# Optimization experiments

Hardware: AMD Instinct MI355X
Metric: run time of the kernel (lower is better)

## Reference

```python
import jax, jax.numpy as jnp
import numpy as np

NEG_SLOPE = 0.2  # PyG GATConv default LeakyReLU slope


def gat_layer(x, src, dst, W, a_src, a_dst, bias, num_nodes, heads, out_ch, concat):
    # x: [N, in], W: [in, heads*out_ch], a_src/a_dst: [heads, out_ch]
    h = (x @ W).reshape(num_nodes, heads, out_ch)          # [N,H,C]
    alpha_s = jnp.sum(h * a_src, axis=-1)                  # [N,H]
    alpha_d = jnp.sum(h * a_dst, axis=-1)                  # [N,H]
    e = jax.nn.leaky_relu(alpha_s[src] + alpha_d[dst], NEG_SLOPE)  # [E,H]
    # softmax over incoming edges of each destination node
    e_max = jax.ops.segment_max(e, dst, num_segments=num_nodes)   # [N,H]
    e_exp = jnp.exp(e - e_max[dst])                        # [E,H]
    denom = jax.ops.segment_sum(e_exp, dst, num_segments=num_nodes)  # [N,H]
    alpha = e_exp / denom[dst]                             # [E,H]
    msg = h[src] * alpha[:, :, None]                       # [E,H,C]
    out = jax.ops.segment_sum(msg, dst, num_segments=num_nodes)     # [N,H,C]
    if concat:
        out = out.reshape(num_nodes, heads * out_ch)
    else:
        out = out.mean(axis=1)
    return out + bias


def setup_inputs() -> dict:
    key = jax.random.key(0)
    ks = jax.random.split(key, 12)
    N, E = 50000, 800000
    IN, HID, OUT, H = 128, 32, 64, 4
    x = jax.random.normal(ks[0], (N, IN), dtype=jnp.float32)
    edge_index = jax.random.randint(ks[1], (2, E), 0, N, dtype=jnp.int32)
    s = 1.0 / np.sqrt(IN)
    W1 = jax.random.normal(ks[2], (IN, H * HID), dtype=jnp.float32) * s
    a_src1 = jax.random.normal(ks[3], (H, HID), dtype=jnp.float32) * 0.1
    a_dst1 = jax.random.normal(ks[4], (H, HID), dtype=jnp.float32) * 0.1
    b1 = jnp.zeros((H * HID,), dtype=jnp.float32)
    s2 = 1.0 / np.sqrt(H * HID)
    W2 = jax.random.normal(ks[5], (H * HID, OUT), dtype=jnp.float32) * s2
    a_src2 = jax.random.normal(ks[6], (1, OUT), dtype=jnp.float32) * 0.1
    a_dst2 = jax.random.normal(ks[7], (1, OUT), dtype=jnp.float32) * 0.1
    b2 = jnp.zeros((OUT,), dtype=jnp.float32)
    return {"x": x, "edge_index": edge_index, "W1": W1, "a_src1": a_src1,
            "a_dst1": a_dst1, "b1": b1, "W2": W2, "a_src2": a_src2,
            "a_dst2": a_dst2, "b2": b2}


def reference(x, edge_index, W1, a_src1, a_dst1, b1, W2, a_src2, a_dst2, b2):
    N = x.shape[0]
    src, dst = edge_index[0], edge_index[1]
    h = gat_layer(x, src, dst, W1, a_src1, a_dst1, b1, N, heads=4, out_ch=32, concat=True)
    h = jax.nn.elu(h)
    # dropout is identity in eval / p=0.0
    out = gat_layer(h, src, dst, W2, a_src2, a_dst2, b2, N, heads=1, out_ch=64, concat=False)
    return out
```

## Files before the change

### kernel.cpp

```cpp
#include <hip/hip_runtime.h>

#define C1 128
#define C2 64
#define CAP 96

typedef __attribute__((ext_vector_type(8))) _Float16 half8;
typedef __attribute__((ext_vector_type(2))) _Float16 half2v;
typedef __attribute__((ext_vector_type(2))) __fp16  fp16x2;
typedef __attribute__((ext_vector_type(4))) float floatx4;

__device__ __forceinline__ float lrelu(float v) { return v > 0.f ? v : 0.2f * v; }

__device__ __forceinline__ unsigned pk2h(float a, float b) {
    union { fp16x2 p; unsigned u; } c;
    c.p = __builtin_amdgcn_cvt_pkrtz(a, b);
    return c.u;
}

__global__ __launch_bounds__(256)
void gemm1_mfma_kernel(const float* __restrict__ x, const float* __restrict__ W1,
                       const float* __restrict__ asrc, const float* __restrict__ adst,
                       unsigned* __restrict__ h1d,
                       float* __restrict__ as1, float* __restrict__ ad1,
                       int* __restrict__ cursor, int N) {
    for (int i = blockIdx.x * 256 + threadIdx.x; i < N; i += gridDim.x * 256)
        cursor[i] = 0;

    __shared__ __align__(16) unsigned short Bs[128 * 136];
    for (int i = threadIdx.x; i < 128 * 64; i += 256) {
        int col = i & 127;
        int k = (i >> 7) * 2;
        *(unsigned*)&Bs[col * 136 + k] = pk2h(W1[k * 128 + col], W1[(k + 1) * 128 + col]);
    }
    __syncthreads();

    const int lane = threadIdx.x & 63, ww = threadIdx.x >> 6;
    const int quad = lane >> 4, l16 = lane & 15;
    const int nodeBase = blockIdx.x * 64 + ww * 16;
    int arow = nodeBase + l16;
    if (arow >= N) arow = N - 1;
    const float* xp = x + (size_t)arow * C1 + quad * 8;
    half8 afr[4];
#pragma unroll
    for (int kk = 0; kk < 4; ++kk) {
        float4 a0 = *(const float4*)(xp + kk * 32);
        float4 a1 = *(const float4*)(xp + kk * 32 + 4);
        union { half8 v; unsigned u[4]; } fr;
        fr.u[0] = pk2h(a0.x, a0.y);
        fr.u[1] = pk2h(a0.z, a0.w);
        fr.u[2] = pk2h(a1.x, a1.y);
        fr.u[3] = pk2h(a1.z, a1.w);
        afr[kk] = fr.v;
    }

#pragma unroll
    for (int h = 0; h < 4; ++h) {
        floatx4 accL = {0.f, 0.f, 0.f, 0.f};
        floatx4 accH = {0.f, 0.f, 0.f, 0.f};
        const int colL = h * 32 + l16;
        const int colH = colL + 16;
        const unsigned short* bL = &Bs[colL * 136 + quad * 8];
        const unsigned short* bH = &Bs[colH * 136 + quad * 8];
#pragma unroll
        for (int kk = 0; kk < 4; ++kk) {
            half8 bfrL = *(const half8*)(bL + kk * 32);
            half8 bfrH = *(const half8*)(bH + kk * 32);
            accL = __builtin_amdgcn_mfma_f32_16x16x32_f16(afr[kk], bfrL, accL, 0, 0, 0);
            accH = __builtin_amdgcn_mfma_f32_16x16x32_f16(afr[kk], bfrH, accH, 0, 0, 0);
        }
#pragma unroll
        for (int reg = 0; reg < 4; ++reg) {
            int node = nodeBase + quad * 4 + reg;
            if (node < N) h1d[(size_t)node * 64 + h * 16 + l16] = pk2h(accL[reg], accH[reg]);
        }
        float avL = asrc[colL], dvL = adst[colL];
        float avH = asrc[colH], dvH = adst[colH];
#pragma unroll
        for (int reg = 0; reg < 4; ++reg) {
            float ts = accL[reg] * avL + accH[reg] * avH;
            float td = accL[reg] * dvL + accH[reg] * dvH;
#pragma unroll
            for (int o = 1; o < 16; o <<= 1) {
                ts += __shfl_xor(ts, o, 64);
                td += __shfl_xor(td, o, 64);
            }
            if (l16 == 0) {
                int node = nodeBase + quad * 4 + reg;
                if (node < N) {
                    as1[node * 4 + h] = ts;
                    ad1[node * 4 + h] = td;
                }
            }
        }
    }
}

__global__ __launch_bounds__(256)
void fill_kernel(const int* __restrict__ ei, int* __restrict__ cursor,
                 int* __restrict__ csrc, int N, int E) {
    const int part = blockIdx.x & 7;
    const int bIdx = blockIdx.x >> 3;
    const int bpp  = gridDim.x >> 3;
    const int lo = (int)(((long)N * part) >> 3);
    const int hi = (int)(((long)N * (part + 1)) >> 3);

    const int E4 = ((E & 3) == 0) ? (E >> 2) : 0;
    const int4* d4 = (const int4*)(ei + E);
    const int4* s4 = (const int4*)ei;
    for (int q = bIdx * 256 + threadIdx.x; q < E4; q += bpp * 256) {
        int4 dv = d4[q];
        int4 sv = s4[q];
        int dd[4] = {dv.x, dv.y, dv.z, dv.w};
        int ss[4] = {sv.x, sv.y, sv.z, sv.w};
        int pos[4];
        bool act[4];
#pragma unroll
        for (int i = 0; i < 4; ++i) {
            act[i] = (dd[i] >= lo) & (dd[i] < hi) & ((unsigned)ss[i] < (unsigned)N);
            pos[i] = act[i] ? atomicAdd(&cursor[dd[i]], 1) : 0;
        }
#pragma unroll
        for (int i = 0; i < 4; ++i)
            if (act[i] && pos[i] < CAP) csrc[dd[i] * CAP + pos[i]] = ss[i];
    }
    for (int e = E4 * 4 + bIdx * 256 + threadIdx.x; e < E; e += bpp * 256) {
        int dd = ei[E + e];
        if (dd < lo || dd >= hi) continue;
        int ss = ei[e];
        if ((unsigned)ss >= (unsigned)N) continue;
        int pp = atomicAdd(&cursor[dd], 1);
        if (pp < CAP) csrc[dd * CAP + pp] = ss;
    }
}

__global__ __launch_bounds__(256)
void msg1_csr_kernel(const int* __restrict__ cursor, const int* __restrict__ csrc,
                     const unsigned* __restrict__ h1u, const float* __restrict__ as1,
                     const float* __restrict__ ad1, const float* __restrict__ b1,
                     unsigned* __restrict__ out1, int N) {
    __shared__ float ws[4][64];
    const int wid = threadIdx.x >> 6;
    const int d = blockIdx.x * 4 + wid;
    if (d >= N) return;
    const int lane = threadIdx.x & 63;
    const int e16 = lane & 15;
    const int head = lane >> 4;
    int dg = cursor[d]; if (dg > CAP) dg = CAP;
    const int base = d * CAP;
    const float wadh = ad1[d * 4 + head];
    float accx = 0.f, accy = 0.f, sumw = 0.f;
    for (int jj = 0; jj < dg; jj += 16) {
        int idx = jj + e16;
        if (idx >= dg) idx = dg - 1;
        const int myS = csrc[base + idx];
        unsigned rv[16];
#pragma unroll
        for (int k = 0; k < 16; ++k) {
            int s = __builtin_amdgcn_readlane(myS, k);
            rv[k] = h1u[(unsigned)s * 64u + (unsigned)lane];
        }
        float w = 0.f;
        if (jj + e16 < dg)
            w = __expf(lrelu(as1[myS * 4 + head] + wadh));
        ws[wid][lane] = w;
#pragma unroll
        for (int j = 0; j < 4; ++j) {
            float4 wf = ((const float4*)&ws[wid][head * 16])[j];
            union { unsigned u; half2v p; } c0, c1, c2, c3;
            c0.u = rv[4 * j + 0]; c1.u = rv[4 * j + 1];
            c2.u = rv[4 * j + 2]; c3.u = rv[4 * j + 3];
            sumw += (wf.x + wf.y) + (wf.z + wf.w);
            accx += wf.x * (float)c0.p[0]; accy += wf.x * (float)c0.p[1];
            accx += wf.y * (float)c1.p[0]; accy += wf.y * (float)c1.p[1];
            accx += wf.z * (float)c2.p[0]; accy += wf.z * (float)c2.p[1];
            accx += wf.w * (float)c3.p[0]; accy += wf.w * (float)c3.p[1];
        }
    }
    float inv = (sumw > 0.f) ? 1.f / sumw : 0.f;
    float rx = accx * inv + b1[32 * head + e16];
    float ry = accy * inv + b1[32 * head + e16 + 16];
    rx = rx > 0.f ? rx : expm1f(rx);
    ry = ry > 0.f ? ry : expm1f(ry);
    out1[(size_t)d * 64 + lane] = pk2h(rx, ry);
}

__global__ __launch_bounds__(256)
void gemm2_mfma_kernel(const unsigned short* __restrict__ h2, const float* __restrict__ W2,
                       const float* __restrict__ asrc, const float* __restrict__ adst,
                       unsigned* __restrict__ g2d, float* __restrict__ as2,
                       float* __restrict__ ad2, int N) {
    __shared__ __align__(16) unsigned short Bs[64 * 136];
    for (int i = threadIdx.x; i < 64 * 64; i += 256) {
        int col = i & 63;
        int p = i >> 6;
        int k0 = 32 * (p >> 4) + (p & 15);
        *(unsigned*)&Bs[col * 136 + 2 * p] = pk2h(W2[k0 * 64 + col], W2[(k0 + 16) * 64 + col]);
    }
    __syncthreads();

    const int lane = threadIdx.x & 63, ww = threadIdx.x >> 6;
    const int quad = lane >> 4, l16 = lane & 15;
    const int nodeBase = blockIdx.x * 64 + ww * 16;
    int arow = nodeBase + l16;
    if (arow >= N) arow = N - 1;
    const unsigned short* xp = h2 + (size_t)arow * C1 + quad * 8;
    half8 afr[4];
#pragma unroll
    for (int kk = 0; kk < 4; ++kk)
        afr[kk] = *(const half8*)(xp + kk * 32);

    float sacc[4] = {0.f,0.f,0.f,0.f}, dacc[4] = {0.f,0.f,0.f,0.f};
#pragma unroll
    for (int ctp = 0; ctp < 2; ++ctp) {
        floatx4 accL = {0.f, 0.f, 0.f, 0.f};
        floatx4 accH = {0.f, 0.f, 0.f, 0.f};
        const int colL = ctp * 16 + l16;
        const int colH = colL + 32;
        const unsigned short* bL = &Bs[colL * 136 + quad * 8];
        const unsigned short* bH = &Bs[colH * 136 + quad * 8];
#pragma unroll
        for (int kk = 0; kk < 4; ++kk) {
            half8 bfrL = *(const half8*)(bL + kk * 32);
            half8 bfrH = *(const half8*)(bH + kk * 32);
            accL = __builtin_amdgcn_mfma_f32_16x16x32_f16(afr[kk], bfrL, accL, 0, 0, 0);
            accH = __builtin_amdgcn_mfma_f32_16x16x32_f16(afr[kk], bfrH, accH, 0, 0, 0);
        }
#pragma unroll
        for (int reg = 0; reg < 4; ++reg) {
            int node = nodeBase + quad * 4 + reg;
            if (node < N) g2d[(size_t)node * 32 + colL] = pk2h(accL[reg], accH[reg]);
        }
        float avL = asrc[colL], dvL = adst[colL];
        float avH = asrc[colH], dvH = adst[colH];
#pragma unroll
        for (int reg = 0; reg < 4; ++reg) {
            sacc[reg] += accL[reg] * avL + accH[reg] * avH;
            dacc[reg] += accL[reg] * dvL + accH[reg] * dvH;
        }
    }
#pragma unroll
    for (int reg = 0; reg < 4; ++reg) {
        float ts = sacc[reg], td = dacc[reg];
#pragma unroll
        for (int o = 1; o < 16; o <<= 1) {
            ts += __shfl_xor(ts, o, 64);
            td += __shfl_xor(td, o, 64);
        }
        if (l16 == 0) {
            int node = nodeBase + quad * 4 + reg;
            if (node < N) { as2[node] = ts; ad2[node] = td; }
        }
    }
}

__global__ __launch_bounds__(256)
void msg2_csr_kernel(const int* __restrict__ cursor, const int* __restrict__ csrc,
                     const unsigned* __restrict__ g2u, const float* __restrict__ as2,
                     const float* __restrict__ ad2, const float* __restrict__ b2,
                     float* __restrict__ yf, int N) {
    __shared__ float wsm[4][32];
    __shared__ int   ssm[4][32];
    const int wid = threadIdx.x >> 6;
    const int d = blockIdx.x * 4 + wid;
    if (d >= N) return;
    const int lane = threadIdx.x & 63;
    const int half = lane >> 5;
    const int l32 = lane & 31;
    int dg = cursor[d]; if (dg > CAP) dg = CAP;
    const int base = d * CAP;
    const float add = ad2[d];
    float accx = 0.f, accy = 0.f, sumw = 0.f;
    for (int jj = 0; jj < dg; jj += 32) {
        int idx = jj + l32;
        if (idx >= dg) idx = dg - 1;
        const int myS = csrc[base + idx];
        float w = 0.f;
        if (jj + l32 < dg) w = __expf(lrelu(as2[myS] + add));
        ssm[wid][l32] = myS;
        wsm[wid][l32] = w;
        int4 s0 = ((const int4*)&ssm[wid][half * 16])[0];
        int4 s1 = ((const int4*)&ssm[wid][half * 16])[1];
        int4 s2 = ((const int4*)&ssm[wid][half * 16])[2];
        int4 s3 = ((const int4*)&ssm[wid][half * 16])[3];
        int ss[16] = {s0.x, s0.y, s0.z, s0.w, s1.x, s1.y, s1.z, s1.w,
                      s2.x, s2.y, s2.z, s2.w, s3.x, s3.y, s3.z, s3.w};
        unsigned rv[16];
#pragma unroll
        for (int k = 0; k < 16; ++k)
            rv[k] = g2u[(unsigned)ss[k] * 32u + (unsigned)l32];
#pragma unroll
        for (int j = 0; j < 4; ++j) {
            float4 wf = ((const float4*)&wsm[wid][half * 16])[j];
            union { unsigned u; half2v p; } c0, c1, c2, c3;
            c0.u = rv[4 * j + 0]; c1.u = rv[4 * j + 1];
            c2.u = rv[4 * j + 2]; c3.u = rv[4 * j + 3];
            sumw += (wf.x + wf.y) + (wf.z + wf.w);
            accx += wf.x * (float)c0.p[0]; accy += wf.x * (float)c0.p[1];
            accx += wf.y * (float)c1.p[0]; accy += wf.y * (float)c1.p[1];
            accx += wf.z * (float)c2.p[0]; accy += wf.z * (float)c2.p[1];
            accx += wf.w * (float)c3.p[0]; accy += wf.w * (float)c3.p[1];
        }
    }
    accx += __shfl_xor(accx, 32, 64);
    accy += __shfl_xor(accy, 32, 64);
    sumw += __shfl_xor(sumw, 32, 64);
    if (half == 0) {
        float inv = (sumw > 0.f) ? 1.f / sumw : 0.f;
        yf[(size_t)d * 64 + l32]      = accx * inv + b2[l32];
        yf[(size_t)d * 64 + 32 + l32] = accy * inv + b2[l32 + 32];
    }
}

extern "C" void kernel_launch(void* const* d_in, const int* in_sizes, int n_in,
                              void* d_out, int out_size, void* d_ws, size_t ws_size,
                              hipStream_t stream) {
    const float* x    = (const float*)d_in[0];
    const int*   ei   = (const int*)d_in[1];
    const float* W1   = (const float*)d_in[2];
    const float* a_s1 = (const float*)d_in[3];
    const float* a_d1 = (const float*)d_in[4];
    const float* b1   = (const float*)d_in[5];
    const float* W2   = (const float*)d_in[6];
    const float* a_s2 = (const float*)d_in[7];
    const float* a_d2 = (const float*)d_in[8];
    const float* b2   = (const float*)d_in[9];

    const int N = in_sizes[0] / C1;
    const int E = in_sizes[1] / 2;

    auto align16 = [](size_t v) { return (v + 15) & ~(size_t)15; };
    const size_t RF   = 16;
    const size_t RCUR = align16((size_t)N * 4);
    const size_t RSRC = align16((size_t)N * CAP * 4);
    const size_t R1   = align16((size_t)N * C1 * 4);
    const size_t R2   = align16((size_t)N * 8 * 4);

    char* base = (char*)d_ws;
    int*  cursor = (int*)(base + RF);
    int*  csrc   = (int*)(base + RF + RCUR);
    char* R1p = base + RF + RCUR + RSRC;
    char* R2p = R1p + R1;
    char* R4p = R2p + R2;
    (void)ws_size;

    unsigned* h1 = (unsigned*)R1p;
    unsigned* g2 = (unsigned*)R1p;
    float* as1 = (float*)R2p;
    float* ad1 = as1 + (size_t)N * 4;
    float* as2 = (float*)R2p;
    float* ad2 = as2 + N;
    unsigned* out1 = (unsigned*)R4p;

    const int nbTile = (N + 63) / 64;
    const int nbWave4 = (N + 3) / 4;

    gemm1_mfma_kernel<<<nbTile, 256, 0, stream>>>(x, W1, a_s1, a_d1, h1, as1, ad1, cursor, N);
    fill_kernel<<<2048, 256, 0, stream>>>(ei, cursor, csrc, N, E);
    msg1_csr_kernel<<<nbWave4, 256, 0, stream>>>(cursor, csrc, (const unsigned*)h1,
        as1, ad1, b1, out1, N);
    gemm2_mfma_kernel<<<nbTile, 256, 0, stream>>>((const unsigned short*)out1, W2,
        a_s2, a_d2, g2, as2, ad2, N);
    msg2_csr_kernel<<<nbWave4, 256, 0, stream>>>(cursor, csrc, (const unsigned*)g2,
        as2, ad2, b2, (float*)d_out, N);
}
```

Baseline: 226.1 us.

## Fuse layer-2 projection into msg1 kernel using fdot2 and shared W2

Removes the separate gemm2 MFMA kernel and computes each node's 64-wide layer-2 projection plus attention logits at the end of msg1, using packed half dot products against a swizzled W2 table in shared memory. This avoids writing and re-reading the intermediate hidden features and one kernel launch. In exchange every 4-node block re-stages and converts all of W2 into LDS, adding global loads and shared memory pressure, and the matmul moves from MFMA to scalar fdot2.

```diff
diff --git a/kernel.cpp b/kernel.cpp
--- a/kernel.cpp
+++ b/kernel.cpp
@@ -15,6 +15,9 @@
     union { fp16x2 p; unsigned u; } c;
     c.p = __builtin_amdgcn_cvt_pkrtz(a, b);
     return c.u;
+}
+__device__ __forceinline__ half2v u2h(unsigned v) {
+    union { unsigned u; half2v h; } c; c.u = v; return c.h;
 }
 
 __global__ __launch_bounds__(256)
@@ -137,8 +140,22 @@
 void msg1_csr_kernel(const int* __restrict__ cursor, const int* __restrict__ csrc,
                      const unsigned* __restrict__ h1u, const float* __restrict__ as1,
                      const float* __restrict__ ad1, const float* __restrict__ b1,
-                     unsigned* __restrict__ out1, int N) {
+                     const float* __restrict__ W2, const float* __restrict__ a_s2,
+                     const float* __restrict__ a_d2,
+                     unsigned* __restrict__ g2d, float* __restrict__ as2,
+                     float* __restrict__ ad2, int N) {
     __shared__ float ws[4][64];
+    __shared__ unsigned h2s[4][64];
+    __shared__ __align__(16) unsigned W2Ls[64][64];
+    for (int i = threadIdx.x; i < 64 * 64; i += 256) {
+        int c = i >> 6, t = i & 63;
+        int bs = t >> 2, j = t & 3;
+        int kp = 4 * (bs ^ (c & 15)) + j;
+        int k0 = 32 * (kp >> 4) + (kp & 15);
+        W2Ls[c][t] = pk2h(W2[k0 * 64 + c], W2[(k0 + 16) * 64 + c]);
+    }
+    __syncthreads();
+
     const int wid = threadIdx.x >> 6;
     const int d = blockIdx.x * 4 + wid;
     if (d >= N) return;
@@ -181,76 +198,28 @@
     float ry = accy * inv + b1[32 * head + e16 + 16];
     rx = rx > 0.f ? rx : expm1f(rx);
     ry = ry > 0.f ? ry : expm1f(ry);
-    out1[(size_t)d * 64 + lane] = pk2h(rx, ry);
-}
-
-__global__ __launch_bounds__(256)
-void gemm2_mfma_kernel(const unsigned short* __restrict__ h2, const float* __restrict__ W2,
-                       const float* __restrict__ asrc, const float* __restrict__ adst,
-                       unsigned* __restrict__ g2d, float* __restrict__ as2,
-                       float* __restrict__ ad2, int N) {
-    __shared__ __align__(16) unsigned short Bs[64 * 136];
-    for (int i = threadIdx.x; i < 64 * 64; i += 256) {
-        int col = i & 63;
-        int p = i >> 6;
-        int k0 = 32 * (p >> 4) + (p & 15);
-        *(unsigned*)&Bs[col * 136 + 2 * p] = pk2h(W2[k0 * 64 + col], W2[(k0 + 16) * 64 + col]);
-    }
-    __syncthreads();
-
-    const int lane = threadIdx.x & 63, ww = threadIdx.x >> 6;
-    const int quad = lane >> 4, l16 = lane & 15;
-    const int nodeBase = blockIdx.x * 64 + ww * 16;
-    int arow = nodeBase + l16;
-    if (arow >= N) arow = N - 1;
-    const unsigned short* xp = h2 + (size_t)arow * C1 + quad * 8;
-    half8 afr[4];
-#pragma unroll
-    for (int kk = 0; kk < 4; ++kk)
-        afr[kk] = *(const half8*)(xp + kk * 32);
-
-    float sacc[4] = {0.f,0.f,0.f,0.f}, dacc[4] = {0.f,0.f,0.f,0.f};
-#pragma unroll
-    for (int ctp = 0; ctp < 2; ++ctp) {
-        floatx4 accL = {0.f, 0.f, 0.f, 0.f};
-        floatx4 accH = {0.f, 0.f, 0.f, 0.f};
-        const int colL = ctp * 16 + l16;
-        const int colH = colL + 32;
-        const unsigned short* bL = &Bs[colL * 136 + quad * 8];
-        const unsigned short* bH = &Bs[colH * 136 + quad * 8];
-#pragma unroll
-        for (int kk = 0; kk < 4; ++kk) {
-            half8 bfrL = *(const half8*)(bL + kk * 32);
-            half8 bfrH = *(const half8*)(bH + kk * 32);
-            accL = __builtin_amdgcn_mfma_f32_16x16x32_f16(afr[kk], bfrL, accL, 0, 0, 0);
-            accH = __builtin_amdgcn_mfma_f32_16x16x32_f16(afr[kk], bfrH, accH, 0, 0, 0);
-        }
-#pragma unroll
-        for (int reg = 0; reg < 4; ++reg) {
-            int node = nodeBase + quad * 4 + reg;
-            if (node < N) g2d[(size_t)node * 32 + colL] = pk2h(accL[reg], accH[reg]);
-        }
-        float avL = asrc[colL], dvL = adst[colL];
-        float avH = asrc[colH], dvH = adst[colH];
-#pragma unroll
-        for (int reg = 0; reg < 4; ++reg) {
-            sacc[reg] += accL[reg] * avL + accH[reg] * avH;
-            dacc[reg] += accL[reg] * dvL + accH[reg] * dvH;
-        }
-    }
-#pragma unroll
-    for (int reg = 0; reg < 4; ++reg) {
-        float ts = sacc[reg], td = dacc[reg];
-#pragma unroll
-        for (int o = 1; o < 16; o <<= 1) {
-            ts += __shfl_xor(ts, o, 64);
-            td += __shfl_xor(td, o, 64);
-        }
-        if (l16 == 0) {
-            int node = nodeBase + quad * 4 + reg;
-            if (node < N) { as2[node] = ts; ad2[node] = td; }
-        }
-    }
+
+    h2s[wid][lane] = pk2h(rx, ry);
+    float acc = 0.f;
+#pragma unroll
+    for (int b = 0; b < 16; ++b) {
+        uint4 hq = *(const uint4*)&h2s[wid][b * 4];
+        uint4 wq = *(const uint4*)&W2Ls[lane][4 * (b ^ (lane & 15))];
+        acc = __builtin_amdgcn_fdot2(u2h(hq.x), u2h(wq.x), acc, false);
+        acc = __builtin_amdgcn_fdot2(u2h(hq.y), u2h(wq.y), acc, false);
+        acc = __builtin_amdgcn_fdot2(u2h(hq.z), u2h(wq.z), acc, false);
+        acc = __builtin_amdgcn_fdot2(u2h(hq.w), u2h(wq.w), acc, false);
+    }
+    float ts = acc * a_s2[lane];
+    float td = acc * a_d2[lane];
+#pragma unroll
+    for (int o = 1; o < 64; o <<= 1) {
+        ts += __shfl_xor(ts, o, 64);
+        td += __shfl_xor(td, o, 64);
+    }
+    if (lane == 0) { as2[d] = ts; ad2[d] = td; }
+    float accO = __shfl_xor(acc, 32, 64);
+    if (lane < 32) g2d[(size_t)d * 32 + lane] = pk2h(acc, accO);
 }
 
 __global__ __launch_bounds__(256)
@@ -344,12 +313,11 @@
     (void)ws_size;
 
     unsigned* h1 = (unsigned*)R1p;
-    unsigned* g2 = (unsigned*)R1p;
     float* as1 = (float*)R2p;
     float* ad1 = as1 + (size_t)N * 4;
-    float* as2 = (float*)R2p;
+    unsigned* g2 = (unsigned*)R4p;
+    float* as2 = (float*)(R4p + align16((size_t)N * 32 * 4));
     float* ad2 = as2 + N;
-    unsigned* out1 = (unsigned*)R4p;
 
     const int nbTile = (N + 63) / 64;
     const int nbWave4 = (N + 3) / 4;
@@ -357,9 +325,7 @@
     gemm1_mfma_kernel<<<nbTile, 256, 0, stream>>>(x, W1, a_s1, a_d1, h1, as1, ad1, cursor, N);
     fill_kernel<<<2048, 256, 0, stream>>>(ei, cursor, csrc, N, E);
     msg1_csr_kernel<<<nbWave4, 256, 0, stream>>>(cursor, csrc, (const unsigned*)h1,
-        as1, ad1, b1, out1, N);
-    gemm2_mfma_kernel<<<nbTile, 256, 0, stream>>>((const unsigned short*)out1, W2,
-        a_s2, a_d2, g2, as2, ad2, N);
+        as1, ad1, b1, W2, a_s2, a_d2, g2, as2, ad2, N);
     msg2_csr_kernel<<<nbWave4, 256, 0, stream>>>(cursor, csrc, (const unsigned*)g2,
         as2, ad2, b2, (float*)d_out, N);
 }
```

After: 382.4 us. 69.2% more time.
